# Kernel tuning notes

Measured on AMD Instinct MI355X. Metric: run time of the kernel, lower is better.

The kernel has to match this reference:

```python
import jax, jax.numpy as jnp
import numpy as np

DIM = 128
NUM_HEADS = 8
HEAD_DIM = DIM // NUM_HEADS
SCALE = HEAD_DIM ** -0.5


def _attn_branch(xs, Wq, bq, Wp, bp):
    # xs: (N, L, C) batch of sequences; Q=K=V=q (per the module)
    N, L, C = xs.shape
    q = xs @ Wq + bq                                   # (N, L, C)
    q = q.reshape(N, L, NUM_HEADS, HEAD_DIM).transpose(0, 2, 1, 3)  # (N, h, L, d)
    qs = q * SCALE
    attn = jax.nn.softmax(jnp.einsum('nhld,nhmd->nhlm', qs, qs), axis=-1)
    out = jnp.einsum('nhlm,nhmd->nhld', attn, q)       # (N, h, L, d)
    out = out.transpose(0, 2, 1, 3).reshape(N, L, C)
    return out @ Wp + bp


def setup_inputs() -> dict:
    key = jax.random.key(0)
    ks = jax.random.split(key, 12)
    B, C, D, H, W = 1, DIM, 31, 32, 32
    s = 0.02
    return {
        'x': jax.random.normal(ks[0], (B, C, D, H, W), jnp.float32),
        'Wq_spec': jax.random.normal(ks[1], (C, C), jnp.float32) * s,
        'bq_spec': jnp.zeros((C,), jnp.float32),
        'Wp_spec': jax.random.normal(ks[2], (C, C), jnp.float32) * s,
        'bp_spec': jnp.zeros((C,), jnp.float32),
        'Wq_spat': jax.random.normal(ks[3], (C, C), jnp.float32) * s,
        'bq_spat': jnp.zeros((C,), jnp.float32),
        'Wp_spat': jax.random.normal(ks[4], (C, C), jnp.float32) * s,
        'bp_spat': jnp.zeros((C,), jnp.float32),
        'Wg': jax.random.normal(ks[5], (2 * C, C), jnp.float32) * s,
        'bg': jnp.zeros((C,), jnp.float32),
    }


def reference(x, Wq_spec, bq_spec, Wp_spec, bp_spec,
              Wq_spat, bq_spat, Wp_spat, bp_spat, Wg, bg):
    B, C, D, H, W = x.shape
    # ---- spectral branch: sequences of length D per spatial position ----
    x_spec = x.transpose(0, 3, 4, 2, 1).reshape(B * H * W, D, C)
    out_spec = _attn_branch(x_spec, Wq_spec, bq_spec, Wp_spec, bp_spec)
    out_spectral = out_spec.reshape(B, H, W, D, C).transpose(0, 4, 3, 1, 2)  # (B,C,D,H,W)
    # ---- spatial branch: sequences of length H*W per band ----
    x_spat = x.transpose(0, 2, 3, 4, 1).reshape(B * D, H * W, C)
    out_spat = _attn_branch(x_spat, Wq_spat, bq_spat, Wp_spat, bp_spat)
    out_spatial = out_spat.reshape(B, D, H, W, C).transpose(0, 4, 1, 2, 3)   # (B,C,D,H,W)
    # ---- sigmoid-gated fusion (global average pooled gate) ----
    gi = jnp.concatenate([
        out_spectral.mean(axis=(2, 3, 4)),
        out_spatial.mean(axis=(2, 3, 4)),
    ], axis=-1)                                          # (B, 2C)
    gate = jax.nn.sigmoid(gi @ Wg + bg)[:, :, None, None, None]  # (B,C,1,1,1)
    return gate * out_spectral + (1.0 - gate) * out_spatial
```

## Files before the change

### kernel.cpp

```cpp
#include <hip/hip_runtime.h>
#include <cstddef>

#define CC 128
#define NH 8
#define HD 16
#define DDIM 31
#define HWW 1024
#define TOK 31744
#define SCALE2 0.0625f

typedef __attribute__((ext_vector_type(4))) short  short4v;
typedef __attribute__((ext_vector_type(4))) float  float4v;

__device__ inline unsigned bf16rne(float f) {
    unsigned u = __float_as_uint(f);
    return (u + 0x7fffu + ((u >> 16) & 1u)) >> 16;
}
__device__ inline float bf2f(unsigned h) { return __uint_as_float(h << 16); }

__device__ inline unsigned packsplit(float v) {
    unsigned h = bf16rne(v);
    unsigned l = bf16rne(v - bf2f(h));
    return h | (l << 16);
}
__device__ inline uint2 pack_hi4(uint4 p) {
    return make_uint2((p.x & 0xffffu) | (p.y << 16),
                      (p.z & 0xffffu) | (p.w << 16));
}
__device__ inline uint2 pack_lo4(uint4 p) {
    return make_uint2((p.x >> 16) | (p.y & 0xffff0000u),
                      (p.z >> 16) | (p.w & 0xffff0000u));
}

__device__ inline void load_wfrags(const float* __restrict__ W, int co0, int l,
                                   int quad, short4v* ah, short4v* al)
{
#pragma unroll
    for (int k8 = 0; k8 < 8; ++k8) {
#pragma unroll
        for (int j = 0; j < 4; ++j) {
            float w = W[(size_t)(k8 * 16 + quad * 4 + j) * CC + co0 + l];
            unsigned h = bf16rne(w);
            ah[k8][j] = (short)h;
            al[k8][j] = (short)bf16rne(w - bf2f(h));
        }
    }
}

#define AST 132

__global__ __launch_bounds__(512, 2) void qproj_kernel(
    const float* __restrict__ x,
    const float* __restrict__ Wq1, const float* __restrict__ Wq2,
    const float* __restrict__ bq1, const float* __restrict__ bq2,
    unsigned* __restrict__ q1p, unsigned* __restrict__ q2p,
    float* __restrict__ sums)
{
    __shared__ ushort sbuf[2 * CC * AST];
    ushort* Ahi = sbuf;
    ushort* Alo = sbuf + CC * AST;
    unsigned* S = (unsigned*)sbuf;
    const int tid = threadIdx.x;
    const int t0  = blockIdx.x * 128;
    if (blockIdx.x == 0 && tid < 2 * CC) sums[tid] = 0.f;

    for (int i = tid; i < CC * 128 / 4; i += 512) {
        int t4 = i & 31, ci = i >> 5;
        float4 v = *(const float4*)&x[(size_t)ci * TOK + t0 + t4 * 4];
        float xv[4] = {v.x, v.y, v.z, v.w};
#pragma unroll
        for (int e = 0; e < 4; ++e) {
            unsigned h = bf16rne(xv[e]);
            unsigned lw = bf16rne(xv[e] - bf2f(h));
            Ahi[(t4 * 4 + e) * AST + ci] = (ushort)h;
            Alo[(t4 * 4 + e) * AST + ci] = (ushort)lw;
        }
    }
    __syncthreads();

    const int lane = tid & 63;
    const int l    = lane & 15;
    const int quad = lane >> 4;
    const int co0  = (tid >> 6) * 16;

    short4v ah[2][8], al[2][8];
    load_wfrags(Wq1, co0, l, quad, ah[0], al[0]);
    load_wfrags(Wq2, co0, l, quad, ah[1], al[1]);
    float4v acc[2][8];
#pragma unroll
    for (int br = 0; br < 2; ++br)
#pragma unroll
        for (int nt = 0; nt < 8; ++nt) acc[br][nt] = (float4v){0.f, 0.f, 0.f, 0.f};
#pragma unroll
    for (int k8 = 0; k8 < 8; ++k8) {
#pragma unroll
        for (int nt = 0; nt < 8; ++nt) {
            short4v bh = *(const short4v*)&Ahi[(nt * 16 + l) * AST + k8 * 16 + quad * 4];
            short4v bl = *(const short4v*)&Alo[(nt * 16 + l) * AST + k8 * 16 + quad * 4];
            acc[0][nt] = __builtin_amdgcn_mfma_f32_16x16x16bf16_1k(ah[0][k8], bh, acc[0][nt], 0, 0, 0);
            acc[0][nt] = __builtin_amdgcn_mfma_f32_16x16x16bf16_1k(ah[0][k8], bl, acc[0][nt], 0, 0, 0);
            acc[0][nt] = __builtin_amdgcn_mfma_f32_16x16x16bf16_1k(al[0][k8], bh, acc[0][nt], 0, 0, 0);
            acc[1][nt] = __builtin_amdgcn_mfma_f32_16x16x16bf16_1k(ah[1][k8], bh, acc[1][nt], 0, 0, 0);
            acc[1][nt] = __builtin_amdgcn_mfma_f32_16x16x16bf16_1k(ah[1][k8], bl, acc[1][nt], 0, 0, 0);
            acc[1][nt] = __builtin_amdgcn_mfma_f32_16x16x16bf16_1k(al[1][k8], bh, acc[1][nt], 0, 0, 0);
        }
    }

    for (int branch = 0; branch < 2; ++branch) {
        const float* bq = branch ? bq2 : bq1;
        unsigned* op    = branch ? q2p : q1p;
        float4 bv = *(const float4*)&bq[co0 + quad * 4];
        float bb[4] = {bv.x, bv.y, bv.z, bv.w};
        __syncthreads();
#pragma unroll
        for (int nt = 0; nt < 8; ++nt) {
#pragma unroll
            for (int reg = 0; reg < 4; ++reg)
                S[(nt * 16 + l) * AST + co0 + quad * 4 + reg] =
                    packsplit(acc[branch][nt][reg] + bb[reg]);
        }
        __syncthreads();
        for (int i = tid; i < 128 * 32; i += 512) {
            int t = i >> 5, c4 = i & 31;
            uint4 pv = *(const uint4*)&S[t * AST + c4 * 4];
            *(uint4*)&op[(size_t)(t0 + t) * CC + c4 * 4] = pv;
        }
    }
}

#define QS2 132
#define QSS 20
#define QTP 1044
__global__ __launch_bounds__(1024, 4) void attn_kernel(
    unsigned* __restrict__ q1p, unsigned* __restrict__ q2p,
    float* __restrict__ sums)
{
    __shared__ __align__(16) ushort smem[HWW * QSS + HD * QTP];
    __shared__ float fsum[CC];
    const int tid  = threadIdx.x;
    const int lane = tid & 63;
    const int l    = lane & 15;
    const int quad = lane >> 4;
    const float k2 = SCALE2 * 1.44269504f;
    const short4v onesb = {(short)0x3F80, (short)0x3F80, (short)0x3F80, (short)0x3F80};
    if (tid < CC) fsum[tid] = 0.f;

    {
        const int d = blockIdx.x >> 3, h = blockIdx.x & 7;
        ushort* Qs  = smem;
        ushort* QTs = smem + HWW * QSS;
        const size_t base = (size_t)d * HWW * CC + h * HD;

        for (int i = tid; i < HWW * 4; i += 1024) {
            int row = i >> 2, q4 = i & 3;
            uint4 p = *(const uint4*)&q2p[base + (size_t)row * CC + q4 * 4];
            *(uint2*)&Qs[row * QSS + q4 * 4] = pack_hi4(p);
            QTs[(q4 * 4 + 0) * QTP + row] = (ushort)p.x;
            QTs[(q4 * 4 + 1) * QTP + row] = (ushort)p.y;
            QTs[(q4 * 4 + 2) * QTP + row] = (ushort)p.z;
            QTs[(q4 * 4 + 3) * QTP + row] = (ushort)p.w;
        }
        __syncthreads();

        const int Rw = (tid >> 6) * 64;
        short4v qf[4];
#pragma unroll
        for (int lt = 0; lt < 4; ++lt) {
            short4v raw = *(short4v*)&Qs[(Rw + lt * 16 + l) * QSS + quad * 4];
            short4v sc;
#pragma unroll
            for (int e = 0; e < 4; ++e) {
                float f = bf2f((unsigned)(ushort)raw[e]) * k2;
                sc[e] = (short)bf16rne(f);
            }
            qf[lt] = sc;
        }

        float4v acc[4], accs[4];
#pragma unroll
        for (int lt = 0; lt < 4; ++lt) {
            acc[lt]  = (float4v){0.f, 0.f, 0.f, 0.f};
            accs[lt] = (float4v){0.f, 0.f, 0.f, 0.f};
        }

#pragma unroll 2
        for (int mt = 0; mt < 64; ++mt) {
            const int m0 = mt * 16;
            short4v ka = *(short4v*)&Qs[(m0 + l) * QSS + quad * 4];
            short4v vb = *(short4v*)&QTs[l * QTP + m0 + quad * 4];
#pragma unroll
            for (int lt = 0; lt < 4; ++lt) {
                float4v s = __builtin_amdgcn_mfma_f32_16x16x16bf16_1k(
                    ka, qf[lt], (float4v){0.f, 0.f, 0.f, 0.f}, 0, 0, 0);
                unsigned u0 = __float_as_uint(__builtin_amdgcn_exp2f(s[0]));
                unsigned u1 = __float_as_uint(__builtin_amdgcn_exp2f(s[1]));
                unsigned u2 = __float_as_uint(__builtin_amdgcn_exp2f(s[2]));
                unsigned u3 = __float_as_uint(__builtin_amdgcn_exp2f(s[3]));
                short4v pf;
                pf[0] = (short)(u0 >> 16); pf[1] = (short)(u1 >> 16);
                pf[2] = (short)(u2 >> 16); pf[3] = (short)(u3 >> 16);
                acc[lt]  = __builtin_amdgcn_mfma_f32_16x16x16bf16_1k(vb, pf, acc[lt], 0, 0, 0);
                accs[lt] = __builtin_amdgcn_mfma_f32_16x16x16bf16_1k(onesb, pf, accs[lt], 0, 0, 0);
            }
        }

        float vsum[4] = {0.f, 0.f, 0.f, 0.f};
#pragma unroll
        for (int lt = 0; lt < 4; ++lt) {
            float inv = 1.f / accs[lt][0];
            int token = Rw + lt * 16 + l;
            float v0 = acc[lt][0] * inv, v1 = acc[lt][1] * inv;
            float v2 = acc[lt][2] * inv, v3 = acc[lt][3] * inv;
            uint4 pv;
            pv.x = packsplit(v0); pv.y = packsplit(v1);
            pv.z = packsplit(v2); pv.w = packsplit(v3);
            *(uint4*)&q2p[base + (size_t)token * CC + quad * 4] = pv;
            vsum[0] += v0; vsum[1] += v1; vsum[2] += v2; vsum[3] += v3;
        }
#pragma unroll
        for (int reg = 0; reg < 4; ++reg) {
            float v = vsum[reg];
            v += __shfl_xor(v, 1); v += __shfl_xor(v, 2);
            v += __shfl_xor(v, 4); v += __shfl_xor(v, 8);
            if (l == 0) atomicAdd(&fsum[quad * 4 + reg], v);
        }
        __syncthreads();
        if (tid < HD) atomicAdd(&sums[CC + h * HD + tid], fsum[tid]);
    }

    const int half_id = blockIdx.x >> 1;
    const bool has_job = (blockIdx.x & 1) ? (half_id < 4) : (half_id < 124);
    if (!has_job) return;
    const int job = (blockIdx.x & 1) ? (124 + half_id) : half_id;
    const int hw0 = job * 8;

    __syncthreads();
    if (tid < CC) fsum[tid] = 0.f;

    const int wave = tid >> 6;
    const int hwl  = wave >> 1;
    const int half = wave & 1;
    const int hw   = hw0 + hwl;
    ushort* Q = smem + hwl * (32 * QS2);
    for (int it = 0; it < 8; ++it) {
        int idx = it * 64 + lane;
        int dd = half * 16 + (idx >> 5), c4 = idx & 31;
        if (dd < 31) {
            uint4 p = *(const uint4*)&q1p[((size_t)dd * HWW + hw) * CC + c4 * 4];
            *(uint2*)&Q[dd * QS2 + c4 * 4] = pack_hi4(p);
        }
    }
    if (half) for (int i = lane; i < 128; i += 64) Q[31 * QS2 + i] = 0;
    __syncthreads();

    const int hh = half * 4;
#pragma unroll
    for (int hl = 0; hl < 4; ++hl) {
        const int hc = (hh + hl) * HD;
        short4v qf[2];
        qf[0] = *(const short4v*)&Q[l * QS2 + hc + quad * 4];
        qf[1] = *(const short4v*)&Q[(16 + l) * QS2 + hc + quad * 4];
        short4v va[2];
#pragma unroll
        for (int j = 0; j < 2; ++j)
#pragma unroll
            for (int jj = 0; jj < 4; ++jj)
                va[j][jj] = (short)Q[(j * 16 + quad * 4 + jj) * QS2 + hc + l];

        float4v o[2]   = {(float4v){0.f,0.f,0.f,0.f}, (float4v){0.f,0.f,0.f,0.f}};
        float4v osr[2] = {(float4v){0.f,0.f,0.f,0.f}, (float4v){0.f,0.f,0.f,0.f}};
#pragma unroll
        for (int j = 0; j < 2; ++j) {
#pragma unroll
            for (int i2 = 0; i2 < 2; ++i2) {
                float4v s = __builtin_amdgcn_mfma_f32_16x16x16bf16_1k(
                    qf[j], qf[i2], (float4v){0.f,0.f,0.f,0.f}, 0, 0, 0);
                unsigned u0 = __float_as_uint(__builtin_amdgcn_exp2f(s[0] * k2));
                unsigned u1 = __float_as_uint(__builtin_amdgcn_exp2f(s[1] * k2));
                unsigned u2 = __float_as_uint(__builtin_amdgcn_exp2f(s[2] * k2));
                unsigned u3 = __float_as_uint(__builtin_amdgcn_exp2f(s[3] * k2));
                if (j == 1 && quad == 3) u3 = 0;
                short4v pf;
                pf[0] = (short)(u0 >> 16); pf[1] = (short)(u1 >> 16);
                pf[2] = (short)(u2 >> 16); pf[3] = (short)(u3 >> 16);
                o[i2]   = __builtin_amdgcn_mfma_f32_16x16x16bf16_1k(va[j], pf, o[i2], 0, 0, 0);
                osr[i2] = __builtin_amdgcn_mfma_f32_16x16x16bf16_1k(onesb, pf, osr[i2], 0, 0, 0);
            }
        }
        float vsum[4] = {0.f, 0.f, 0.f, 0.f};
#pragma unroll
        for (int i2 = 0; i2 < 2; ++i2) {
            float inv = 1.f / osr[i2][0];
            int dq = i2 * 16 + l;
            if (dq < 31) {
                uint4 pv;
                float v0 = o[i2][0] * inv, v1 = o[i2][1] * inv;
                float v2 = o[i2][2] * inv, v3 = o[i2][3] * inv;
                pv.x = packsplit(v0); pv.y = packsplit(v1);
                pv.z = packsplit(v2); pv.w = packsplit(v3);
                *(uint4*)&q1p[((size_t)dq * HWW + hw) * CC + hc + quad * 4] = pv;
                vsum[0] += v0; vsum[1] += v1; vsum[2] += v2; vsum[3] += v3;
            }
        }
#pragma unroll
        for (int r = 0; r < 4; ++r) {
            float v = vsum[r];
            v += __shfl_xor(v, 1); v += __shfl_xor(v, 2);
            v += __shfl_xor(v, 4); v += __shfl_xor(v, 8);
            if (l == 0) atomicAdd(&fsum[hc + quad * 4 + r], v);
        }
    }
    __syncthreads();
    if (tid < CC) atomicAdd(&sums[tid], fsum[tid]);
}

__global__ __launch_bounds__(512, 2) void oproj_kernel(
    const unsigned* __restrict__ q1p, const unsigned* __restrict__ q2p,
    const float* __restrict__ Wp1, const float* __restrict__ Wp2,
    const float* __restrict__ bp1, const float* __restrict__ bp2,
    const float* __restrict__ Wg,  const float* __restrict__ bg,
    const float* __restrict__ sums, float* __restrict__ out)
{
    __shared__ ushort sbuf[2 * 64 * AST];
    ushort* Ahi = sbuf;
    ushort* Alo = sbuf + 64 * AST;
    unsigned* S = (unsigned*)sbuf;
    __shared__ float pa[4][CC];
    __shared__ float giv[2 * CC];
    __shared__ float gf[CC];
    const int tid = threadIdx.x;
    const int t0  = blockIdx.x * 64;
    const int lane = tid & 63;
    const int l    = lane & 15;
    const int quad = lane >> 4;
    const int co0  = (tid >> 6) * 16;

    {
        const int part = tid >> 7, c = tid & 127;
        const float* Wp = (part < 2) ? Wp1 : Wp2;
        const float* sp = (part < 2) ? sums : sums + CC;
        const int k0 = (part & 1) * 64;
        float a = 0.f;
        for (int kk = 0; kk < 64; ++kk) {
            int k = k0 + kk;
            a += sp[k] * Wp[(size_t)k * CC + c];
        }
        pa[part][c] = a;
        __syncthreads();
        if (tid < 2 * CC) {
            float m = (tid < CC) ? (pa[0][tid] + pa[1][tid])
                                 : (pa[2][tid - CC] + pa[3][tid - CC]);
            float bb = (tid < CC) ? bp1[tid] : bp2[tid - CC];
            giv[tid] = m * (1.f / (float)TOK) + bb;
        }
        __syncthreads();
        float b = 0.f;
        for (int kk = 0; kk < 64; ++kk) {
            int j = part * 64 + kk;
            b += giv[j] * Wg[(size_t)j * CC + c];
        }
        pa[part][c] = b;
        __syncthreads();
        if (tid < CC)
            gf[tid] = 1.f / (1.f + __expf(-(bg[tid] + pa[0][tid] + pa[1][tid] +
                                           pa[2][tid] + pa[3][tid])));
    }

    float4v acc[2][4];
#pragma unroll
    for (int br = 0; br < 2; ++br)
#pragma unroll
        for (int nt = 0; nt < 4; ++nt) acc[br][nt] = (float4v){0.f, 0.f, 0.f, 0.f};

    for (int br = 0; br < 2; ++br) {
        const unsigned* Ap = br ? q2p : q1p;
        const float*    W  = br ? Wp2 : Wp1;
        short4v ah[8], al[8];
        load_wfrags(W, co0, l, quad, ah, al);
        __syncthreads();
        for (int i = tid; i < 64 * 32; i += 512) {
            int t = i >> 5, c4 = i & 31;
            uint4 p = *(const uint4*)&Ap[(size_t)(t0 + t) * CC + c4 * 4];
            *(uint2*)&Ahi[t * AST + c4 * 4] = pack_hi4(p);
            *(uint2*)&Alo[t * AST + c4 * 4] = pack_lo4(p);
        }
        __syncthreads();
#pragma unroll
        for (int k8 = 0; k8 < 8; ++k8) {
#pragma unroll
            for (int nt = 0; nt < 4; ++nt) {
                short4v bh = *(const short4v*)&Ahi[(nt * 16 + l) * AST + k8 * 16 + quad * 4];
                short4v bl = *(const short4v*)&Alo[(nt * 16 + l) * AST + k8 * 16 + quad * 4];
                acc[br][nt] = __builtin_amdgcn_mfma_f32_16x16x16bf16_1k(ah[k8], bh, acc[br][nt], 0, 0, 0);
                acc[br][nt] = __builtin_amdgcn_mfma_f32_16x16x16bf16_1k(ah[k8], bl, acc[br][nt], 0, 0, 0);
                acc[br][nt] = __builtin_amdgcn_mfma_f32_16x16x16bf16_1k(al[k8], bh, acc[br][nt], 0, 0, 0);
            }
        }
    }

    float4 b1 = *(const float4*)&bp1[co0 + quad * 4];
    float4 b2 = *(const float4*)&bp2[co0 + quad * 4];
    float bb1[4] = {b1.x, b1.y, b1.z, b1.w};
    float bb2[4] = {b2.x, b2.y, b2.z, b2.w};
    float gg[4];
#pragma unroll
    for (int e = 0; e < 4; ++e) gg[e] = gf[co0 + quad * 4 + e];

    __syncthreads();
#pragma unroll
    for (int nt = 0; nt < 4; ++nt) {
        int tl = nt * 16 + l;
#pragma unroll
        for (int reg = 0; reg < 4; ++reg) {
            float v = gg[reg] * (acc[0][nt][reg] + bb1[reg]) +
                      (1.f - gg[reg]) * (acc[1][nt][reg] + bb2[reg]);
            S[(co0 + quad * 4 + reg) * 66 + tl] = __float_as_uint(v);
        }
    }
    __syncthreads();
    for (int i = tid; i < 128 * 32; i += 512) {
        int co = i >> 5, t2 = i & 31;
        uint2 v = *(const uint2*)&S[co * 66 + t2 * 2];
        *(uint2*)&out[(size_t)co * TOK + t0 + t2 * 2] = v;
    }
}

extern "C" void kernel_launch(void* const* d_in, const int* in_sizes, int n_in,
                              void* d_out, int out_size, void* d_ws, size_t ws_size,
                              hipStream_t stream)
{
    const float* x   = (const float*)d_in[0];
    const float* Wq1 = (const float*)d_in[1];
    const float* bq1 = (const float*)d_in[2];
    const float* Wp1 = (const float*)d_in[3];
    const float* bp1 = (const float*)d_in[4];
    const float* Wq2 = (const float*)d_in[5];
    const float* bq2 = (const float*)d_in[6];
    const float* Wp2 = (const float*)d_in[7];
    const float* bp2 = (const float*)d_in[8];
    const float* Wg  = (const float*)d_in[9];
    const float* bg  = (const float*)d_in[10];
    float* out = (float*)d_out;

    unsigned* q1p = (unsigned*)d_ws;
    unsigned* q2p = q1p + (size_t)TOK * CC;
    float*   sums = (float*)(q2p + (size_t)TOK * CC);

    qproj_kernel<<<dim3(248), 512, 0, stream>>>(x, Wq1, Wq2, bq1, bq2,
                                                q1p, q2p, sums);
    attn_kernel<<<dim3(248), 1024, 0, stream>>>(q1p, q2p, sums);
    oproj_kernel<<<dim3(496), 512, 0, stream>>>(q1p, q2p,
                                                Wp1, Wp2, bp1, bp2, Wg, bg,
                                                sums, out);
}
```

Measured before the change: 177.1 us.

## Use 16x16x32 bf16 MFMA in projections, halve qproj tile, pack exp via perm

The Q and output projection GEMMs move from 16x16x16 to 16x16x32 bf16 MFMA instructions with 8-wide fragments, which halves the instruction count for the split-bf16 products. qproj now handles 64 tokens per block instead of 128, doubling the grid and cutting LDS use, and both projection kernels raise their launch-bounds occupancy hint to 4. The LDS row stride changes to 136. In the attention loops, the bf16 truncation of exp results is packed with v_perm instead of per-element shifts. The trade-off is more register pressure at the higher occupancy hint and possible LDS bank conflicts with the new stride.

Result: faster. 173.0 us (-2.3%).

```diff
diff --git a/kernel.cpp b/kernel.cpp
--- a/kernel.cpp
+++ b/kernel.cpp
@@ -8,9 +8,13 @@
 #define HWW 1024
 #define TOK 31744
 #define SCALE2 0.0625f
+#define QTOK 64
 
 typedef __attribute__((ext_vector_type(4))) short  short4v;
+typedef __attribute__((ext_vector_type(8))) short  short8v;
 typedef __attribute__((ext_vector_type(4))) float  float4v;
+typedef __attribute__((ext_vector_type(2))) unsigned uint2v;
+typedef __attribute__((ext_vector_type(8))) __bf16 bf16x8;
 
 __device__ inline unsigned bf16rne(float f) {
     unsigned u = __float_as_uint(f);
@@ -32,40 +36,53 @@
                       (p.z >> 16) | (p.w & 0xffff0000u));
 }
 
-__device__ inline void load_wfrags(const float* __restrict__ W, int co0, int l,
-                                   int quad, short4v* ah, short4v* al)
+__device__ inline short4v pack_pf(unsigned u0, unsigned u1,
+                                  unsigned u2, unsigned u3) {
+    uint2v pd;
+    pd[0] = __builtin_amdgcn_perm(u1, u0, 0x07060302u);
+    pd[1] = __builtin_amdgcn_perm(u3, u2, 0x07060302u);
+    return __builtin_bit_cast(short4v, pd);
+}
+
+__device__ inline float4v mfma32(short8v a, short8v b, float4v c) {
+    return __builtin_amdgcn_mfma_f32_16x16x32_bf16(
+        __builtin_bit_cast(bf16x8, a), __builtin_bit_cast(bf16x8, b), c, 0, 0, 0);
+}
+
+__device__ inline void load_wfrags32(const float* __restrict__ W, int co0, int l,
+                                     int quad, short8v* ah, short8v* al)
 {
 #pragma unroll
-    for (int k8 = 0; k8 < 8; ++k8) {
-#pragma unroll
-        for (int j = 0; j < 4; ++j) {
-            float w = W[(size_t)(k8 * 16 + quad * 4 + j) * CC + co0 + l];
+    for (int k4 = 0; k4 < 4; ++k4) {
+#pragma unroll
+        for (int j = 0; j < 8; ++j) {
+            float w = W[(size_t)(k4 * 32 + quad * 8 + j) * CC + co0 + l];
             unsigned h = bf16rne(w);
-            ah[k8][j] = (short)h;
-            al[k8][j] = (short)bf16rne(w - bf2f(h));
-        }
-    }
-}
-
-#define AST 132
-
-__global__ __launch_bounds__(512, 2) void qproj_kernel(
+            ah[k4][j] = (short)h;
+            al[k4][j] = (short)bf16rne(w - bf2f(h));
+        }
+    }
+}
+
+#define AST 136
+
+__global__ __launch_bounds__(512, 4) void qproj_kernel(
     const float* __restrict__ x,
     const float* __restrict__ Wq1, const float* __restrict__ Wq2,
     const float* __restrict__ bq1, const float* __restrict__ bq2,
     unsigned* __restrict__ q1p, unsigned* __restrict__ q2p,
     float* __restrict__ sums)
 {
-    __shared__ ushort sbuf[2 * CC * AST];
+    __shared__ ushort sbuf[2 * QTOK * AST];
     ushort* Ahi = sbuf;
-    ushort* Alo = sbuf + CC * AST;
+    ushort* Alo = sbuf + QTOK * AST;
     unsigned* S = (unsigned*)sbuf;
     const int tid = threadIdx.x;
-    const int t0  = blockIdx.x * 128;
+    const int t0  = blockIdx.x * QTOK;
     if (blockIdx.x == 0 && tid < 2 * CC) sums[tid] = 0.f;
 
-    for (int i = tid; i < CC * 128 / 4; i += 512) {
-        int t4 = i & 31, ci = i >> 5;
+    for (int i = tid; i < CC * QTOK / 4; i += 512) {
+        int t4 = i & 15, ci = i >> 4;
         float4 v = *(const float4*)&x[(size_t)ci * TOK + t0 + t4 * 4];
         float xv[4] = {v.x, v.y, v.z, v.w};
 #pragma unroll
@@ -83,26 +100,26 @@
     const int quad = lane >> 4;
     const int co0  = (tid >> 6) * 16;
 
-    short4v ah[2][8], al[2][8];
-    load_wfrags(Wq1, co0, l, quad, ah[0], al[0]);
-    load_wfrags(Wq2, co0, l, quad, ah[1], al[1]);
-    float4v acc[2][8];
+    short8v ah[2][4], al[2][4];
+    load_wfrags32(Wq1, co0, l, quad, ah[0], al[0]);
+    load_wfrags32(Wq2, co0, l, quad, ah[1], al[1]);
+    float4v acc[2][4];
 #pragma unroll
     for (int br = 0; br < 2; ++br)
 #pragma unroll
-        for (int nt = 0; nt < 8; ++nt) acc[br][nt] = (float4v){0.f, 0.f, 0.f, 0.f};
-#pragma unroll
-    for (int k8 = 0; k8 < 8; ++k8) {
-#pragma unroll
-        for (int nt = 0; nt < 8; ++nt) {
-            short4v bh = *(const short4v*)&Ahi[(nt * 16 + l) * AST + k8 * 16 + quad * 4];
-            short4v bl = *(const short4v*)&Alo[(nt * 16 + l) * AST + k8 * 16 + quad * 4];
-            acc[0][nt] = __builtin_amdgcn_mfma_f32_16x16x16bf16_1k(ah[0][k8], bh, acc[0][nt], 0, 0, 0);
-            acc[0][nt] = __builtin_amdgcn_mfma_f32_16x16x16bf16_1k(ah[0][k8], bl, acc[0][nt], 0, 0, 0);
-            acc[0][nt] = __builtin_amdgcn_mfma_f32_16x16x16bf16_1k(al[0][k8], bh, acc[0][nt], 0, 0, 0);
-            acc[1][nt] = __builtin_amdgcn_mfma_f32_16x16x16bf16_1k(ah[1][k8], bh, acc[1][nt], 0, 0, 0);
-            acc[1][nt] = __builtin_amdgcn_mfma_f32_16x16x16bf16_1k(ah[1][k8], bl, acc[1][nt], 0, 0, 0);
-            acc[1][nt] = __builtin_amdgcn_mfma_f32_16x16x16bf16_1k(al[1][k8], bh, acc[1][nt], 0, 0, 0);
+        for (int nt = 0; nt < 4; ++nt) acc[br][nt] = (float4v){0.f, 0.f, 0.f, 0.f};
+#pragma unroll
+    for (int k4 = 0; k4 < 4; ++k4) {
+#pragma unroll
+        for (int nt = 0; nt < 4; ++nt) {
+            short8v bh = *(const short8v*)&Ahi[(nt * 16 + l) * AST + k4 * 32 + quad * 8];
+            short8v bl = *(const short8v*)&Alo[(nt * 16 + l) * AST + k4 * 32 + quad * 8];
+            acc[0][nt] = mfma32(ah[0][k4], bh, acc[0][nt]);
+            acc[0][nt] = mfma32(ah[0][k4], bl, acc[0][nt]);
+            acc[0][nt] = mfma32(al[0][k4], bh, acc[0][nt]);
+            acc[1][nt] = mfma32(ah[1][k4], bh, acc[1][nt]);
+            acc[1][nt] = mfma32(ah[1][k4], bl, acc[1][nt]);
+            acc[1][nt] = mfma32(al[1][k4], bh, acc[1][nt]);
         }
     }
 
@@ -113,14 +130,14 @@
         float bb[4] = {bv.x, bv.y, bv.z, bv.w};
         __syncthreads();
 #pragma unroll
-        for (int nt = 0; nt < 8; ++nt) {
+        for (int nt = 0; nt < 4; ++nt) {
 #pragma unroll
             for (int reg = 0; reg < 4; ++reg)
                 S[(nt * 16 + l) * AST + co0 + quad * 4 + reg] =
                     packsplit(acc[branch][nt][reg] + bb[reg]);
         }
         __syncthreads();
-        for (int i = tid; i < 128 * 32; i += 512) {
+        for (int i = tid; i < QTOK * 32; i += 512) {
             int t = i >> 5, c4 = i & 31;
             uint4 pv = *(const uint4*)&S[t * AST + c4 * 4];
             *(uint4*)&op[(size_t)(t0 + t) * CC + c4 * 4] = pv;
@@ -196,9 +213,7 @@
                 unsigned u1 = __float_as_uint(__builtin_amdgcn_exp2f(s[1]));
                 unsigned u2 = __float_as_uint(__builtin_amdgcn_exp2f(s[2]));
                 unsigned u3 = __float_as_uint(__builtin_amdgcn_exp2f(s[3]));
-                short4v pf;
-                pf[0] = (short)(u0 >> 16); pf[1] = (short)(u1 >> 16);
-                pf[2] = (short)(u2 >> 16); pf[3] = (short)(u3 >> 16);
+                short4v pf = pack_pf(u0, u1, u2, u3);
                 acc[lt]  = __builtin_amdgcn_mfma_f32_16x16x16bf16_1k(vb, pf, acc[lt], 0, 0, 0);
                 accs[lt] = __builtin_amdgcn_mfma_f32_16x16x16bf16_1k(onesb, pf, accs[lt], 0, 0, 0);
             }
@@ -280,9 +295,7 @@
                 unsigned u2 = __float_as_uint(__builtin_amdgcn_exp2f(s[2] * k2));
                 unsigned u3 = __float_as_uint(__builtin_amdgcn_exp2f(s[3] * k2));
                 if (j == 1 && quad == 3) u3 = 0;
-                short4v pf;
-                pf[0] = (short)(u0 >> 16); pf[1] = (short)(u1 >> 16);
-                pf[2] = (short)(u2 >> 16); pf[3] = (short)(u3 >> 16);
+                short4v pf = pack_pf(u0, u1, u2, u3);
                 o[i2]   = __builtin_amdgcn_mfma_f32_16x16x16bf16_1k(va[j], pf, o[i2], 0, 0, 0);
                 osr[i2] = __builtin_amdgcn_mfma_f32_16x16x16bf16_1k(onesb, pf, osr[i2], 0, 0, 0);
             }
@@ -314,7 +327,7 @@
     if (tid < CC) atomicAdd(&sums[tid], fsum[tid]);
 }
 
-__global__ __launch_bounds__(512, 2) void oproj_kernel(
+__global__ __launch_bounds__(512, 4) void oproj_kernel(
     const unsigned* __restrict__ q1p, const unsigned* __restrict__ q2p,
     const float* __restrict__ Wp1, const float* __restrict__ Wp2,
     const float* __restrict__ bp1, const float* __restrict__ bp2,
@@ -375,8 +388,8 @@
     for (int br = 0; br < 2; ++br) {
         const unsigned* Ap = br ? q2p : q1p;
         const float*    W  = br ? Wp2 : Wp1;
-        short4v ah[8], al[8];
-        load_wfrags(W, co0, l, quad, ah, al);
+        short8v ah[4], al[4];
+        load_wfrags32(W, co0, l, quad, ah, al);
         __syncthreads();
         for (int i = tid; i < 64 * 32; i += 512) {
             int t = i >> 5, c4 = i & 31;
@@ -386,14 +399,14 @@
         }
         __syncthreads();
 #pragma unroll
-        for (int k8 = 0; k8 < 8; ++k8) {
+        for (int k4 = 0; k4 < 4; ++k4) {
 #pragma unroll
             for (int nt = 0; nt < 4; ++nt) {
-                short4v bh = *(const short4v*)&Ahi[(nt * 16 + l) * AST + k8 * 16 + quad * 4];
-                short4v bl = *(const short4v*)&Alo[(nt * 16 + l) * AST + k8 * 16 + quad * 4];
-                acc[br][nt] = __builtin_amdgcn_mfma_f32_16x16x16bf16_1k(ah[k8], bh, acc[br][nt], 0, 0, 0);
-                acc[br][nt] = __builtin_amdgcn_mfma_f32_16x16x16bf16_1k(ah[k8], bl, acc[br][nt], 0, 0, 0);
-                acc[br][nt] = __builtin_amdgcn_mfma_f32_16x16x16bf16_1k(al[k8], bh, acc[br][nt], 0, 0, 0);
+                short8v bh = *(const short8v*)&Ahi[(nt * 16 + l) * AST + k4 * 32 + quad * 8];
+                short8v bl = *(const short8v*)&Alo[(nt * 16 + l) * AST + k4 * 32 + quad * 8];
+                acc[br][nt] = mfma32(ah[k4], bh, acc[br][nt]);
+                acc[br][nt] = mfma32(ah[k4], bl, acc[br][nt]);
+                acc[br][nt] = mfma32(al[k4], bh, acc[br][nt]);
             }
         }
     }
@@ -442,12 +455,13 @@
     const float* bg  = (const float*)d_in[10];
     float* out = (float*)d_out;
 
+    const size_t plane = (size_t)TOK * CC;
     unsigned* q1p = (unsigned*)d_ws;
-    unsigned* q2p = q1p + (size_t)TOK * CC;
-    float*   sums = (float*)(q2p + (size_t)TOK * CC);
-
-    qproj_kernel<<<dim3(248), 512, 0, stream>>>(x, Wq1, Wq2, bq1, bq2,
-                                                q1p, q2p, sums);
+    unsigned* q2p = q1p + plane;
+    float*   sums = (float*)(q2p + plane);
+
+    qproj_kernel<<<dim3(TOK / QTOK), 512, 0, stream>>>(x, Wq1, Wq2, bq1, bq2,
+                                                       q1p, q2p, sums);
     attn_kernel<<<dim3(248), 1024, 0, stream>>>(q1p, q2p, sums);
     oproj_kernel<<<dim3(496), 512, 0, stream>>>(q1p, q2p,
                                                 Wp1, Wp2, bp1, bp2, Wg, bg,
```
